# Performance work log

Measured on AMD Instinct MI355X. Metric: run time of the kernel, lower is better.

The kernel has to match this reference:

```python
import jax, jax.numpy as jnp
import numpy as np

N_BEST = 50          # hypotheses per utterance segment
NUM_SEG = 1_000_000  # number of utterance segments
TOTAL = N_BEST * NUM_SEG


def setup_inputs() -> dict:
    key = jax.random.key(0)
    scores = jax.random.normal(key, (TOTAL,), dtype=jnp.float32)
    # per-segment n-best counts; sum(nBestIndex) == len(scores)
    nBestIndex = jnp.full((NUM_SEG,), N_BEST, dtype=jnp.int32)
    return {"scores": scores, "nBestIndex": nBestIndex}


def reference(scores, nBestIndex):
    # Segmented (ragged) softmax: softmax within each contiguous n-best group.
    # Equivalent to the torch loop with log_score=False, fused into one pass.
    num_seg = nBestIndex.shape[0]
    total = scores.shape[0]
    # segment id for each score element
    seg = jnp.repeat(jnp.arange(num_seg, dtype=jnp.int32), nBestIndex,
                     total_repeat_length=total)
    # numerically stable segmented softmax
    seg_max = jax.ops.segment_max(scores, seg, num_segments=num_seg)
    exps = jnp.exp(scores - seg_max[seg])
    seg_sum = jax.ops.segment_sum(exps, seg, num_segments=num_seg)
    return exps / seg_sum[seg]
```

## Files before the change

### kernel.cpp

```cpp
#include <hip/hip_runtime.h>
#include <math.h>


#define GSEG   16
#define SPG    4
#define SBLOCK 256
#define SEGS_B ((SBLOCK / GSEG) * SPG)
#define LDS_FLOATS 3328

__global__ __launch_bounds__(256) void scan_local_kernel(
    const int* __restrict__ counts, int n_seg,
    int* __restrict__ local_scan, int* __restrict__ block_sums) {
    __shared__ int sm[256];
    const int t = threadIdx.x;
    const int g = blockIdx.x * 256 + t;
    const int v = (g < n_seg) ? counts[g] : 0;
    sm[t] = v;
    __syncthreads();
    for (int off = 1; off < 256; off <<= 1) {
        int y = (t >= off) ? sm[t - off] : 0;
        __syncthreads();
        sm[t] += y;
        __syncthreads();
    }
    if (g < n_seg) local_scan[g] = sm[t] - v;
    if (t == 255) block_sums[blockIdx.x] = sm[255];
}

__global__ __launch_bounds__(256) void scan_bsums_kernel(
    int* __restrict__ bsum, int nb) {
    __shared__ int sm[256];
    const int t = threadIdx.x;
    const int per = (nb + 255) >> 8;
    const int beg = t * per;
    const int end = (beg + per < nb) ? beg + per : nb;
    int tot = 0;
    for (int j = beg; j < end; ++j) tot += bsum[j];
    sm[t] = tot;
    __syncthreads();
    for (int off = 1; off < 256; off <<= 1) {
        int y = (t >= off) ? sm[t - off] : 0;
        __syncthreads();
        sm[t] += y;
        __syncthreads();
    }
    int run = sm[t] - tot;
    for (int j = beg; j < end; ++j) {
        int v = bsum[j];
        bsum[j] = run;
        run += v;
    }
}

__global__ __launch_bounds__(SBLOCK) void seg_softmax_kernel(
    const float* __restrict__ scores,
    const int* __restrict__ local_scan, const int* __restrict__ bsum,
    float* __restrict__ out, int n_seg, int total) {
    __shared__ float sm[LDS_FLOATS];
    __shared__ int starts[SEGS_B + 1];

    const int tid  = threadIdx.x;
    const int seg0 = blockIdx.x * SEGS_B;

    if (tid <= SEGS_B) {
        const int s = seg0 + tid;
        starts[tid] = (s < n_seg) ? (local_scan[s] + bsum[s >> 8]) : total;
    }

    const int base  = local_scan[seg0] + bsum[seg0 >> 8];
    const int eseg  = seg0 + SEGS_B;
    const int bend  = (eseg < n_seg) ? (local_scan[eseg] + bsum[eseg >> 8]) : total;
    const int span  = bend - base;

    if (span <= LDS_FLOATS && (base & 3) == 0) {
        const float4* __restrict__ src = (const float4*)(scores + base);
        const int nvec = span >> 2;
        for (int i = tid; i < nvec; i += SBLOCK)
            ((float4*)sm)[i] = src[i];
        for (int i = (nvec << 2) + tid; i < span; i += SBLOCK)
            sm[i] = scores[base + i];
        __syncthreads();

        const int p   = tid & (GSEG - 1);
        const int grp = tid >> 4;

        int st[SPG], c[SPG];
        #pragma unroll
        for (int q = 0; q < SPG; ++q) {
            const int ls = grp * SPG + q;
            st[q] = starts[ls] - base;
            c[q]  = starts[ls + 1] - starts[ls];
        }

        #pragma unroll
        for (int q = 0; q < SPG; ++q) {
            if (c[q] <= 0) continue;
            if (c[q] <= 4 * GSEG) {
                float v0 = -INFINITY, v1 = -INFINITY, v2 = -INFINITY, v3 = -INFINITY;
                const int i0 = p, i1 = p + GSEG, i2 = p + 2 * GSEG, i3 = p + 3 * GSEG;
                if (i0 < c[q]) v0 = sm[st[q] + i0];
                if (i1 < c[q]) v1 = sm[st[q] + i1];
                if (i2 < c[q]) v2 = sm[st[q] + i2];
                if (i3 < c[q]) v3 = sm[st[q] + i3];

                float m = fmaxf(fmaxf(v0, v1), fmaxf(v2, v3));
                #pragma unroll
                for (int off = 1; off < GSEG; off <<= 1)
                    m = fmaxf(m, __shfl_xor(m, off, GSEG));

                const float e0 = __expf(v0 - m);
                const float e1 = __expf(v1 - m);
                const float e2 = __expf(v2 - m);
                const float e3 = __expf(v3 - m);
                float s = (e0 + e1) + (e2 + e3);
                #pragma unroll
                for (int off = 1; off < GSEG; off <<= 1)
                    s += __shfl_xor(s, off, GSEG);

                const float inv = __builtin_amdgcn_rcpf(s);
                if (i0 < c[q]) sm[st[q] + i0] = e0 * inv;
                if (i1 < c[q]) sm[st[q] + i1] = e1 * inv;
                if (i2 < c[q]) sm[st[q] + i2] = e2 * inv;
                if (i3 < c[q]) sm[st[q] + i3] = e3 * inv;
            } else {
                float m = -INFINITY;
                for (int j = p; j < c[q]; j += GSEG)
                    m = fmaxf(m, sm[st[q] + j]);
                #pragma unroll
                for (int off = 1; off < GSEG; off <<= 1)
                    m = fmaxf(m, __shfl_xor(m, off, GSEG));
                float s = 0.0f;
                for (int j = p; j < c[q]; j += GSEG) {
                    const float e = __expf(sm[st[q] + j] - m);
                    sm[st[q] + j] = e;
                    s += e;
                }
                #pragma unroll
                for (int off = 1; off < GSEG; off <<= 1)
                    s += __shfl_xor(s, off, GSEG);
                const float inv = __builtin_amdgcn_rcpf(s);
                for (int j = p; j < c[q]; j += GSEG)
                    sm[st[q] + j] *= inv;
            }
        }
        __syncthreads();

        float4* __restrict__ dst = (float4*)(out + base);
        for (int i = tid; i < nvec; i += SBLOCK)
            dst[i] = ((const float4*)sm)[i];
        for (int i = (nvec << 2) + tid; i < span; i += SBLOCK)
            out[base + i] = sm[i];
    } else {
        __syncthreads();
        const int p   = tid & (GSEG - 1);
        const int grp = tid >> 4;
        #pragma unroll
        for (int q = 0; q < SPG; ++q) {
            const int ls = grp * SPG + q;
            const int st = starts[ls];
            const int c  = starts[ls + 1] - st;
            if (c <= 0) continue;
            float m = -INFINITY;
            for (int j = p; j < c; j += GSEG)
                m = fmaxf(m, scores[st + j]);
            #pragma unroll
            for (int off = 1; off < GSEG; off <<= 1)
                m = fmaxf(m, __shfl_xor(m, off, GSEG));
            float s = 0.0f;
            for (int j = p; j < c; j += GSEG)
                s += __expf(scores[st + j] - m);
            #pragma unroll
            for (int off = 1; off < GSEG; off <<= 1)
                s += __shfl_xor(s, off, GSEG);
            const float inv = __builtin_amdgcn_rcpf(s);
            for (int j = p; j < c; j += GSEG)
                out[st + j] = __expf(scores[st + j] - m) * inv;
        }
    }
}

extern "C" void kernel_launch(void* const* d_in, const int* in_sizes, int n_in,
                              void* d_out, int out_size, void* d_ws, size_t ws_size,
                              hipStream_t stream) {
    const float* scores = (const float*)d_in[0];
    const int*   counts = (const int*)d_in[1];
    float* out = (float*)d_out;
    const int n_seg = in_sizes[1];
    const int total = in_sizes[0];

    int* local_scan = (int*)d_ws;
    const int nblocksA = (n_seg + 255) / 256;
    int* block_sums = local_scan + n_seg;

    scan_local_kernel<<<nblocksA, 256, 0, stream>>>(counts, n_seg, local_scan, block_sums);
    scan_bsums_kernel<<<1, 256, 0, stream>>>(block_sums, nblocksA);

    const int nblocksC = (n_seg + SEGS_B - 1) / SEGS_B;
    seg_softmax_kernel<<<nblocksC, SBLOCK, 0, stream>>>(
        scores, local_scan, block_sums, out, n_seg, total);
}
```

Baseline: 351.1 us.

## Persistent grid-stride softmax with register prefetch of next span

Turns the segmented softmax kernel into a persistent kernel on a fixed grid of 2048 blocks. Each block strides over 32-segment spans and loads the next span's scores and offsets into registers while it computes the current span from LDS. Spans per block shrink from 64 to 32 segments, with a smaller LDS buffer and launch bounds set for higher occupancy. Each wave writes its own quarter of the output back with only a wave-level wait instead of a block barrier. This aims to hide global load latency at the cost of more registers and added control complexity.

```diff
diff --git a/kernel.cpp b/kernel.cpp
--- a/kernel.cpp
+++ b/kernel.cpp
@@ -3,10 +3,11 @@
 
 
 #define GSEG   16
-#define SPG    4
+#define SPG    2
 #define SBLOCK 256
-#define SEGS_B ((SBLOCK / GSEG) * SPG)
-#define LDS_FLOATS 3328
+#define SEGS_B 32
+#define CAPF   1664
+#define GRID_C 2048
 
 __global__ __launch_bounds__(256) void scan_local_kernel(
     const int* __restrict__ counts, int n_seg,
@@ -52,131 +53,194 @@
     }
 }
 
-__global__ __launch_bounds__(SBLOCK) void seg_softmax_kernel(
+__global__ __launch_bounds__(SBLOCK, 4) void seg_softmax_kernel(
     const float* __restrict__ scores,
     const int* __restrict__ local_scan, const int* __restrict__ bsum,
     float* __restrict__ out, int n_seg, int total) {
-    __shared__ float sm[LDS_FLOATS];
-    __shared__ int starts[SEGS_B + 1];
-
-    const int tid  = threadIdx.x;
-    const int seg0 = blockIdx.x * SEGS_B;
-
-    if (tid <= SEGS_B) {
-        const int s = seg0 + tid;
-        starts[tid] = (s < n_seg) ? (local_scan[s] + bsum[s >> 8]) : total;
-    }
-
-    const int base  = local_scan[seg0] + bsum[seg0 >> 8];
-    const int eseg  = seg0 + SEGS_B;
-    const int bend  = (eseg < n_seg) ? (local_scan[eseg] + bsum[eseg >> 8]) : total;
-    const int span  = bend - base;
-
-    if (span <= LDS_FLOATS && (base & 3) == 0) {
-        const float4* __restrict__ src = (const float4*)(scores + base);
-        const int nvec = span >> 2;
-        for (int i = tid; i < nvec; i += SBLOCK)
-            ((float4*)sm)[i] = src[i];
-        for (int i = (nvec << 2) + tid; i < span; i += SBLOCK)
-            sm[i] = scores[base + i];
-        __syncthreads();
-
-        const int p   = tid & (GSEG - 1);
-        const int grp = tid >> 4;
-
-        int st[SPG], c[SPG];
-        #pragma unroll
-        for (int q = 0; q < SPG; ++q) {
-            const int ls = grp * SPG + q;
-            st[q] = starts[ls] - base;
-            c[q]  = starts[ls + 1] - starts[ls];
-        }
-
-        #pragma unroll
-        for (int q = 0; q < SPG; ++q) {
-            if (c[q] <= 0) continue;
-            if (c[q] <= 4 * GSEG) {
-                float v0 = -INFINITY, v1 = -INFINITY, v2 = -INFINITY, v3 = -INFINITY;
-                const int i0 = p, i1 = p + GSEG, i2 = p + 2 * GSEG, i3 = p + 3 * GSEG;
-                if (i0 < c[q]) v0 = sm[st[q] + i0];
-                if (i1 < c[q]) v1 = sm[st[q] + i1];
-                if (i2 < c[q]) v2 = sm[st[q] + i2];
-                if (i3 < c[q]) v3 = sm[st[q] + i3];
-
-                float m = fmaxf(fmaxf(v0, v1), fmaxf(v2, v3));
-                #pragma unroll
-                for (int off = 1; off < GSEG; off <<= 1)
-                    m = fmaxf(m, __shfl_xor(m, off, GSEG));
-
-                const float e0 = __expf(v0 - m);
-                const float e1 = __expf(v1 - m);
-                const float e2 = __expf(v2 - m);
-                const float e3 = __expf(v3 - m);
-                float s = (e0 + e1) + (e2 + e3);
-                #pragma unroll
-                for (int off = 1; off < GSEG; off <<= 1)
-                    s += __shfl_xor(s, off, GSEG);
-
-                const float inv = __builtin_amdgcn_rcpf(s);
-                if (i0 < c[q]) sm[st[q] + i0] = e0 * inv;
-                if (i1 < c[q]) sm[st[q] + i1] = e1 * inv;
-                if (i2 < c[q]) sm[st[q] + i2] = e2 * inv;
-                if (i3 < c[q]) sm[st[q] + i3] = e3 * inv;
+
+    __shared__ float buf[CAPF];
+    __shared__ int   tab[SEGS_B + 1];
+
+    const int tid    = threadIdx.x;
+    const int stride = gridDim.x;
+    const int nspans = (n_seg + SEGS_B - 1) / SEGS_B;
+
+    int t = blockIdx.x;
+    if (t >= nspans) return;
+
+    #define SEG_START(s) (((s) < n_seg) ? (local_scan[(s)] + bsum[(s) >> 8]) : total)
+
+    const int lane = tid & 63;
+    const int wv   = tid >> 6;
+    const int p    = tid & (GSEG - 1);
+    const int grp  = tid >> 4;
+
+    int curb0 = SEG_START(t * SEGS_B);
+    int curb1 = SEG_START(t * SEGS_B + SEGS_B);
+    int tregA = 0;
+    if (tid <= SEGS_B) tregA = SEG_START(t * SEGS_B + tid);
+    bool fitCur = ((curb1 - curb0) <= CAPF) && ((curb0 & 3) == 0);
+
+    float4 r0, r1;
+    float  rt;
+    if (fitCur) {
+        const int nvec = (curb1 - curb0) >> 2;
+        const int rem  = (curb1 - curb0) & 3;
+        const float4* __restrict__ src = (const float4*)(scores + curb0);
+        if (tid < nvec)          r0 = src[tid];
+        if (tid + SBLOCK < nvec) r1 = src[tid + SBLOCK];
+        if (tid < rem)           rt = scores[curb0 + (nvec << 2) + tid];
+    }
+
+    int tn = t + stride;
+    int nxtb0 = 0, nxtb1 = 0, tregB = 0;
+    if (tn < nspans) {
+        nxtb0 = SEG_START(tn * SEGS_B);
+        nxtb1 = SEG_START(tn * SEGS_B + SEGS_B);
+        if (tid <= SEGS_B) tregB = SEG_START(tn * SEGS_B + tid);
+    }
+
+    while (true) {
+        __syncthreads();
+
+        const int spanf = curb1 - curb0;
+        if (fitCur) {
+            const int nvec = spanf >> 2;
+            const int rem  = spanf & 3;
+            float4* d = (float4*)buf;
+            if (tid < nvec)          d[tid] = r0;
+            if (tid + SBLOCK < nvec) d[tid + SBLOCK] = r1;
+            if (tid < rem)           buf[(nvec << 2) + tid] = rt;
+        }
+        if (tid <= SEGS_B) tab[tid] = tregA;
+        __syncthreads();
+
+        const bool haveNext = (tn < nspans);
+        const bool fitNext  = haveNext &&
+                              ((nxtb1 - nxtb0) <= CAPF) && ((nxtb0 & 3) == 0);
+        if (fitNext) {
+            const int nv2  = (nxtb1 - nxtb0) >> 2;
+            const int rem2 = (nxtb1 - nxtb0) & 3;
+            const float4* __restrict__ src = (const float4*)(scores + nxtb0);
+            if (tid < nv2)          r0 = src[tid];
+            if (tid + SBLOCK < nv2) r1 = src[tid + SBLOCK];
+            if (tid < rem2)         rt = scores[nxtb0 + (nv2 << 2) + tid];
+        }
+        const int tnn = tn + stride;
+        int nnb0 = 0, nnb1 = 0, tregC = 0;
+        if (tnn < nspans) {
+            nnb0 = SEG_START(tnn * SEGS_B);
+            nnb1 = SEG_START(tnn * SEGS_B + SEGS_B);
+            if (tid <= SEGS_B) tregC = SEG_START(tnn * SEGS_B + tid);
+        }
+
+        if (fitCur) {
+            #pragma unroll
+            for (int q = 0; q < SPG; ++q) {
+                const int ls = grp * SPG + q;
+                const int s0 = tab[ls] - curb0;
+                const int c  = tab[ls + 1] - tab[ls];
+                if (c <= 0) continue;
+                if (c <= 4 * GSEG) {
+                    const int i0 = p, i1 = p + GSEG, i2 = p + 2 * GSEG, i3 = p + 3 * GSEG;
+                    float v0 = -INFINITY, v1 = -INFINITY, v2 = -INFINITY, v3 = -INFINITY;
+                    if (i0 < c) v0 = buf[s0 + i0];
+                    if (i1 < c) v1 = buf[s0 + i1];
+                    if (i2 < c) v2 = buf[s0 + i2];
+                    if (i3 < c) v3 = buf[s0 + i3];
+
+                    float m = fmaxf(fmaxf(v0, v1), fmaxf(v2, v3));
+                    #pragma unroll
+                    for (int off = 1; off < GSEG; off <<= 1)
+                        m = fmaxf(m, __shfl_xor(m, off, GSEG));
+
+                    const float e0 = __expf(v0 - m);
+                    const float e1 = __expf(v1 - m);
+                    const float e2 = __expf(v2 - m);
+                    const float e3 = __expf(v3 - m);
+                    float s = (e0 + e1) + (e2 + e3);
+                    #pragma unroll
+                    for (int off = 1; off < GSEG; off <<= 1)
+                        s += __shfl_xor(s, off, GSEG);
+
+                    const float inv = __builtin_amdgcn_rcpf(s);
+                    if (i0 < c) buf[s0 + i0] = e0 * inv;
+                    if (i1 < c) buf[s0 + i1] = e1 * inv;
+                    if (i2 < c) buf[s0 + i2] = e2 * inv;
+                    if (i3 < c) buf[s0 + i3] = e3 * inv;
+                } else {
+                    float m = -INFINITY;
+                    for (int j = p; j < c; j += GSEG)
+                        m = fmaxf(m, buf[s0 + j]);
+                    #pragma unroll
+                    for (int off = 1; off < GSEG; off <<= 1)
+                        m = fmaxf(m, __shfl_xor(m, off, GSEG));
+                    float s = 0.0f;
+                    for (int j = p; j < c; j += GSEG) {
+                        const float e = __expf(buf[s0 + j] - m);
+                        buf[s0 + j] = e;
+                        s += e;
+                    }
+                    #pragma unroll
+                    for (int off = 1; off < GSEG; off <<= 1)
+                        s += __shfl_xor(s, off, GSEG);
+                    const float inv = __builtin_amdgcn_rcpf(s);
+                    for (int j = p; j < c; j += GSEG)
+                        buf[s0 + j] *= inv;
+                }
+            }
+
+            __builtin_amdgcn_wave_barrier();
+            __asm__ __volatile__("s_waitcnt lgkmcnt(0)" ::: "memory");
+            __builtin_amdgcn_sched_barrier(0);
+
+            const int wseg = wv * (SEGS_B / 4);
+            const int ob   = tab[wseg];
+            const int oe   = tab[wseg + (SEGS_B / 4)];
+            const int rel  = ob - curb0;
+            const int len  = oe - ob;
+            if (((ob | rel) & 3) == 0) {
+                const int nv = len >> 2;
+                const int rm = len & 3;
+                float4* __restrict__ dst = (float4*)(out + ob);
+                const float4* __restrict__ s4 = (const float4*)(buf + rel);
+                for (int j = lane; j < nv; j += 64) dst[j] = s4[j];
+                if (lane < rm) out[ob + (nv << 2) + lane] = buf[rel + (nv << 2) + lane];
             } else {
+                for (int j = lane; j < len; j += 64) out[ob + j] = buf[rel + j];
+            }
+        } else {
+            #pragma unroll
+            for (int q = 0; q < SPG; ++q) {
+                const int ls = grp * SPG + q;
+                const int st = tab[ls];
+                const int c  = tab[ls + 1] - st;
+                if (c <= 0) continue;
                 float m = -INFINITY;
-                for (int j = p; j < c[q]; j += GSEG)
-                    m = fmaxf(m, sm[st[q] + j]);
+                for (int j = p; j < c; j += GSEG)
+                    m = fmaxf(m, scores[st + j]);
                 #pragma unroll
                 for (int off = 1; off < GSEG; off <<= 1)
                     m = fmaxf(m, __shfl_xor(m, off, GSEG));
                 float s = 0.0f;
-                for (int j = p; j < c[q]; j += GSEG) {
-                    const float e = __expf(sm[st[q] + j] - m);
-                    sm[st[q] + j] = e;
-                    s += e;
-                }
+                for (int j = p; j < c; j += GSEG)
+                    s += __expf(scores[st + j] - m);
                 #pragma unroll
                 for (int off = 1; off < GSEG; off <<= 1)
                     s += __shfl_xor(s, off, GSEG);
                 const float inv = __builtin_amdgcn_rcpf(s);
-                for (int j = p; j < c[q]; j += GSEG)
-                    sm[st[q] + j] *= inv;
+                for (int j = p; j < c; j += GSEG)
+                    out[st + j] = __expf(scores[st + j] - m) * inv;
             }
         }
-        __syncthreads();
-
-        float4* __restrict__ dst = (float4*)(out + base);
-        for (int i = tid; i < nvec; i += SBLOCK)
-            dst[i] = ((const float4*)sm)[i];
-        for (int i = (nvec << 2) + tid; i < span; i += SBLOCK)
-            out[base + i] = sm[i];
-    } else {
-        __syncthreads();
-        const int p   = tid & (GSEG - 1);
-        const int grp = tid >> 4;
-        #pragma unroll
-        for (int q = 0; q < SPG; ++q) {
-            const int ls = grp * SPG + q;
-            const int st = starts[ls];
-            const int c  = starts[ls + 1] - st;
-            if (c <= 0) continue;
-            float m = -INFINITY;
-            for (int j = p; j < c; j += GSEG)
-                m = fmaxf(m, scores[st + j]);
-            #pragma unroll
-            for (int off = 1; off < GSEG; off <<= 1)
-                m = fmaxf(m, __shfl_xor(m, off, GSEG));
-            float s = 0.0f;
-            for (int j = p; j < c; j += GSEG)
-                s += __expf(scores[st + j] - m);
-            #pragma unroll
-            for (int off = 1; off < GSEG; off <<= 1)
-                s += __shfl_xor(s, off, GSEG);
-            const float inv = __builtin_amdgcn_rcpf(s);
-            for (int j = p; j < c; j += GSEG)
-                out[st + j] = __expf(scores[st + j] - m) * inv;
-        }
-    }
+
+        if (!haveNext) break;
+        t = tn; tn = tnn;
+        curb0 = nxtb0; curb1 = nxtb1; tregA = tregB;
+        nxtb0 = nnb0;  nxtb1 = nnb1;  tregB = tregC;
+        fitCur = fitNext;
+    }
+    #undef SEG_START
 }
 
 extern "C" void kernel_launch(void* const* d_in, const int* in_sizes, int n_in,
@@ -195,7 +259,8 @@
     scan_local_kernel<<<nblocksA, 256, 0, stream>>>(counts, n_seg, local_scan, block_sums);
     scan_bsums_kernel<<<1, 256, 0, stream>>>(block_sums, nblocksA);
 
-    const int nblocksC = (n_seg + SEGS_B - 1) / SEGS_B;
-    seg_softmax_kernel<<<nblocksC, SBLOCK, 0, stream>>>(
+    const int nspans = (n_seg + SEGS_B - 1) / SEGS_B;
+    const int grid   = (nspans < GRID_C) ? nspans : GRID_C;
+    seg_softmax_kernel<<<grid, SBLOCK, 0, stream>>>(
         scores, local_scan, block_sums, out, n_seg, total);
 }
```

Measured after the change: 350.7 us. No clear change (-0.1%).
